# Kernel optimization log

Hardware: AMD Instinct MI355X
Metric: run time of the kernel (lower is better)

Reference implementation:

```python
import jax, jax.numpy as jnp
import numpy as np

# Dimensions
BATCH = 4
NUM_NODE = 20000
NUM_EDGE = 1280000   # avg degree 64
K = 2                # num_rd_kernels
NUM_SEQ = 13         # num_sequence (13 time points -> 12 intervals)
SEQ_IN = 12
RES = 2              # fixed-step Euler substeps per interval (resolution)
TEMP = 1.0           # temperature for gate softmax
NUM_OUT = -12        # num_output_sequence slice


def setup_inputs() -> dict:
    key = jax.random.key(0)
    ks = jax.random.split(key, 6)
    inputs = jax.random.normal(ks[0], (BATCH, 1, NUM_NODE, SEQ_IN), dtype=jnp.float32)
    gate = jax.random.normal(ks[1], (NUM_SEQ - 1, K), dtype=jnp.float32)
    # edge list from adjacency CSV (from/to columns)
    src = jax.random.randint(ks[2], (NUM_EDGE,), 0, NUM_NODE)
    dst = jax.random.randint(ks[3], (NUM_EDGE,), 0, NUM_NODE)
    # learned per-kernel parameters of multi_reaction_diffusion
    w = jax.random.normal(ks[4], (K, NUM_EDGE), dtype=jnp.float32) * 0.1  # edge diffusivity logits
    r = jax.random.normal(ks[5], (K, NUM_NODE), dtype=jnp.float32) * 0.1  # node reaction coeffs
    return {"inputs": inputs, "gate": gate, "w": w, "r": r, "src": src, "dst": dst}


def _dxdt(x, g, w, r, src, dst):
    # x: [B,N]  g: [K]  w: [K,E]  r: [K,N]
    a = jax.nn.sigmoid(w)                                   # [K,E] edge diffusivity
    xs = x[:, src]                                          # [B,E]
    xd = x[:, dst]                                          # [B,E]
    msg = a[:, None, :] * (xs - xd)[None, :, :]             # [K,B,E]
    # scatter-add messages into destination nodes
    diff = jax.ops.segment_sum(jnp.moveaxis(msg, 2, 0), dst, num_segments=NUM_NODE)  # [N,K,B]
    diff = jnp.transpose(diff, (1, 2, 0))                   # [K,B,N]
    react = r[:, None, :] * x[None] * (1.0 - x[None])       # [K,B,N] logistic reaction
    return jnp.einsum('k,kbn->bn', g, diff + react)         # gate-weighted mix of RD kernels


def reference(inputs, gate, w, r, src, dst):
    x0 = inputs[:, 0, :, -1]                                # [B,N]
    dt = 1.0 / (NUM_SEQ - 1)
    h = jnp.float32(dt / RES)
    gates = jax.nn.softmax(gate / TEMP, axis=-1)            # [NUM_SEQ-1, K]

    def interval(x, g):
        def step(xc, _):
            return xc + h * _dxdt(xc, g, w, r, src, dst), None
        x, _ = jax.lax.scan(step, x, None, length=RES)
        return x, x

    _, traj = jax.lax.scan(interval, x0, gates)             # [NUM_SEQ-1, B, N]
    out = jnp.concatenate([x0[None], traj], axis=0)         # [NUM_SEQ, B, N]
    return out[NUM_OUT:]                                    # last 12 horizons
```

## Files before the change

kernel.cpp:

```cpp
#include <hip/hip_runtime.h>
#include <hip/hip_fp16.h>
#include <math.h>

#define NNODE 20000
#define NEDGE 1280000
#define HSTEP (1.0f/24.0f)
#define NBUCK 313
#define CAP   4608
#define EPB   2048
#define NPB   40
#define TPB   320
#define NBLK  (NNODE/NPB)
#define CAPB  2976
#define NGRP  25
#define GSZ   20
#define XSTR  160256

#define GEPI(g)   (32*(g))
#define RCNTI(g)  (32*(25+(g)))
#define XARRI(x)  (32*(50+(x)))
#define XCNTI(x)  (32*(58+(x)))
#define MASTERI   (32*66)
#define RMASTERI  (32*67)

#define AGT __HIP_MEMORY_SCOPE_AGENT

__global__ void rd_init(const float* __restrict__ inp,
                        uint2* __restrict__ xh,
                        int* __restrict__ cursor,
                        int* __restrict__ bar) {
    int n = blockIdx.x * blockDim.x + threadIdx.x;
    if (n < NBUCK) cursor[n] = n * CAP;
    if (n < 2560) bar[n] = 0;
    if (n < NNODE) {
        float x0 = inp[0 * NNODE * 12 + n * 12 + 11];
        float x1 = inp[1 * NNODE * 12 + n * 12 + 11];
        float x2 = inp[2 * NNODE * 12 + n * 12 + 11];
        float x3 = inp[3 * NNODE * 12 + n * 12 + 11];
        __half2 lo = __floats2half2_rn(x0, x1);
        __half2 hi = __floats2half2_rn(x2, x3);
        uint2 st;
        st.x = *(unsigned*)&lo;
        st.y = *(unsigned*)&hi;
        xh[n] = st;
    }
}

__global__ __launch_bounds__(256) void rd_part(const int4* __restrict__ src4,
                                               const int4* __restrict__ dst4,
                                               const float4* __restrict__ w4,
                                               int* __restrict__ cursor,
                                               uint2* __restrict__ rec) {
    __shared__ int h[4][NBUCK];
    __shared__ uint4 cache[EPB / 4];
    int t = threadIdx.x, wv = t >> 6;
    for (int i = t; i < 4 * NBUCK; i += 256) ((int*)h)[i] = 0;
    __syncthreads();
    int q0 = blockIdx.x * (EPB / 4);
    #pragma unroll
    for (int k = 0; k < 2; ++k) {
        int qi = q0 + k * 256 + t;
        int4 d4 = dst4[qi];
        int dd[4] = {d4.x, d4.y, d4.z, d4.w};
        unsigned cc[4];
        #pragma unroll
        for (int u = 0; u < 4; ++u) {
            int rank = atomicAdd(&h[wv][dd[u] >> 6], 1);
            cc[u] = (unsigned)dd[u] | ((unsigned)rank << 15);
        }
        cache[k * 256 + t] = make_uint4(cc[0], cc[1], cc[2], cc[3]);
    }
    __syncthreads();
    for (int i = t; i < NBUCK; i += 256) {
        int c0 = h[0][i], c1 = h[1][i], c2 = h[2][i], c3 = h[3][i];
        int tot = c0 + c1 + c2 + c3;
        int gb = tot ? atomicAdd(&cursor[i], tot) : 0;
        h[0][i] = gb;
        h[1][i] = gb + c0;
        h[2][i] = gb + c0 + c1;
        h[3][i] = gb + c0 + c1 + c2;
    }
    __syncthreads();
    #pragma unroll
    for (int k = 0; k < 2; ++k) {
        int qi = q0 + k * 256 + t;
        int4 s4 = src4[qi];
        float4 wa = w4[qi];
        float4 wb = w4[NEDGE / 4 + qi];
        uint4 c4 = cache[k * 256 + t];
        int ss[4] = {s4.x, s4.y, s4.z, s4.w};
        float fa[4] = {wa.x, wa.y, wa.z, wa.w};
        float fb[4] = {wb.x, wb.y, wb.z, wb.w};
        unsigned cc[4] = {c4.x, c4.y, c4.z, c4.w};
        #pragma unroll
        for (int u = 0; u < 4; ++u) {
            int d = cc[u] & 0x7FFF;
            int rank = (int)(cc[u] >> 15);
            int b = d >> 6;
            int p = h[wv][b] + rank;
            float s0 = 1.0f / (1.0f + expf(-fa[u]));
            float s1 = 1.0f / (1.0f + expf(-fb[u]));
            __half2 hh = __floats2half2_rn(s0, s1);
            uint2 rq;
            rq.x = (unsigned)ss[u] | ((unsigned)(d & 63) << 16);
            rq.y = *(unsigned*)&hh;
            if (p < (b + 1) * CAP) rec[p] = rq;
        }
    }
}

__global__ void rd_bscan(const int* __restrict__ cursor, int* __restrict__ boff) {
    int lane = threadIdx.x;
    int carry = 0;
    #pragma unroll
    for (int c = 0; c < 5; ++c) {
        int i = c * 64 + lane;
        int v = (i < NBUCK) ? (cursor[i] - i * CAP) : 0;
        int incl = v;
        #pragma unroll
        for (int o = 1; o < 64; o <<= 1) {
            int u = __shfl_up(incl, o, 64);
            if (lane >= o) incl += u;
        }
        if (i < NBUCK) boff[i] = carry + incl - v;
        carry += __shfl(incl, 63, 64);
    }
    if (lane == 0) boff[NBUCK] = carry;
}

__global__ __launch_bounds__(512) void rd_bsort(const uint2* __restrict__ rec,
                                                const int* __restrict__ cursor,
                                                const int* __restrict__ boff,
                                                unsigned short* __restrict__ es16,
                                                unsigned* __restrict__ ew32,
                                                int* __restrict__ offsets) {
    __shared__ uint2 rs[CAP];
    __shared__ int h[64], excl[64];
    int b = blockIdx.x;
    int ib = b * CAP;
    int cnt = cursor[b] - ib; if (cnt > CAP) cnt = CAP;
    int ob = boff[b];
    if (threadIdx.x < 64) h[threadIdx.x] = 0;
    __syncthreads();
    for (int i = threadIdx.x; i < cnt; i += 512) {
        uint2 q = rec[ib + i];
        rs[i] = q;
        atomicAdd(&h[(q.x >> 16) & 63], 1);
    }
    __syncthreads();
    if (threadIdx.x < 64) {
        int lane = threadIdx.x;
        int v = h[lane];
        int incl = v;
        #pragma unroll
        for (int o = 1; o < 64; o <<= 1) {
            int u = __shfl_up(incl, o, 64);
            if (lane >= o) incl += u;
        }
        excl[lane] = incl - v;
        int n = b * 64 + lane;
        if (n < NNODE) offsets[n] = ob + excl[lane];
        h[lane] = 0;
    }
    if (b == NBUCK - 1 && threadIdx.x == 0) offsets[NNODE] = NEDGE;
    __syncthreads();
    for (int i = threadIdx.x; i < cnt; i += 512) {
        uint2 q = rs[i];
        int dl = (q.x >> 16) & 63;
        int rank = atomicAdd(&h[dl], 1);
        int p = ob + excl[dl] + rank;
        es16[p] = (unsigned short)(q.x & 0xFFFFu);
        ew32[p] = q.y;
    }
}

__global__ __launch_bounds__(TPB, 3) void rd_run(
        const float* __restrict__ inp, const uint2* __restrict__ x0h,
        char* __restrict__ recb,
        const unsigned short* __restrict__ es16,
        const unsigned* __restrict__ ew32,
        const int* __restrict__ offsets,
        const float* __restrict__ r, const float* __restrict__ gate,
        float* __restrict__ out, int* bar) {
    __shared__ uint2 lrec[CAPB];
    __shared__ int lofs[NPB + 1];
    __shared__ float lgate[24];
    int t = threadIdx.x;
    int n0 = blockIdx.x * NPB;
    if (t <= NPB) lofs[t] = offsets[n0 + t];
    if (t >= 64 && t < 88) lgate[t - 64] = gate[t - 64];
    __syncthreads();
    int ebase = lofs[0];
    int ecnt  = lofs[NPB] - ebase; if (ecnt > CAPB) ecnt = CAPB;
    for (int i = t; i < ecnt; i += TPB)
        lrec[i] = make_uint2((unsigned)es16[ebase + i], ew32[ebase + i]);
    int node = n0 + (t >> 3);
    int sub  = t & 7;
    float r0n = r[node], r1n = r[NNODE + node];
    float4 xreg;
    xreg.x = inp[0 * NNODE * 12 + node * 12 + 11];
    xreg.y = inp[1 * NNODE * 12 + node * 12 + 11];
    xreg.z = inp[2 * NNODE * 12 + node * 12 + 11];
    xreg.w = inp[3 * NNODE * 12 + node * 12 + 11];
    int jb = lofs[t >> 3] - ebase;
    int je = lofs[(t >> 3) + 1] - ebase;
    int grp = blockIdx.x / GSZ;

    int myxcd = 0, nx = 0, nxcd = 0;
    if (t == 0) {
        __builtin_amdgcn_fence(__ATOMIC_ACQUIRE, "agent");
        myxcd = (int)(__builtin_amdgcn_s_getreg(63508) & 0xF);
        __hip_atomic_fetch_add(&bar[XCNTI(myxcd)], 1, __ATOMIC_RELAXED, AGT);
        int rA = __hip_atomic_fetch_add(&bar[RCNTI(grp)], 1, __ATOMIC_RELEASE, AGT);
        if (rA == GSZ - 1) {
            int rm = __hip_atomic_fetch_add(&bar[RMASTERI], 1, __ATOMIC_RELAXED, AGT);
            if (rm == NGRP - 1)
                for (int g = 0; g < NGRP; ++g)
                    __hip_atomic_store(&bar[GEPI(g)], 1, __ATOMIC_RELAXED, AGT);
        }
        while (__hip_atomic_load(&bar[GEPI(grp)], __ATOMIC_RELAXED, AGT) < 1)
            __builtin_amdgcn_s_sleep(2);
        asm volatile("" ::: "memory");
        nx = __hip_atomic_load(&bar[XCNTI(myxcd)], __ATOMIC_RELAXED, AGT);
        for (int x2 = 0; x2 < 8; ++x2)
            nxcd += (__hip_atomic_load(&bar[XCNTI(x2)], __ATOMIC_RELAXED, AGT) > 0);
    }
    __syncthreads();

    float S0 = 0.f, S1 = 0.f;
    for (int j = jb + sub; j < je; j += 8) {
        uint2 q = lrec[j];
        float2 f = __half22float2(*(__half2*)&q.y);
        S0 += f.x; S1 += f.y;
    }
    #pragma unroll
    for (int m = 4; m >= 1; m >>= 1) {
        S0 += __shfl_xor(S0, m, 64);
        S1 += __shfl_xor(S1, m, 64);
    }

    for (int p = 0; p < 24; ++p) {
        int itv = p >> 1;
        float ga = lgate[2 * itv], gb = lgate[2 * itv + 1];
        float g0 = 1.0f / (1.0f + expf(gb - ga));
        float g1 = 1.0f - g0;
        float rc = fmaf(g0, r0n, g1 * r1n);
        float wsum = fmaf(g0, S0, g1 * S1);
        const uint2* xi = p ? (const uint2*)(recb + (size_t)(p - 1) * XSTR) : x0h;
        uint2*       xo = (uint2*)(recb + (size_t)p * XSTR);

        float4 acc = make_float4(0.f, 0.f, 0.f, 0.f);
        int j = jb + sub;
        for (; j + 56 < je; j += 64) {
            uint2 q0 = lrec[j],      q1 = lrec[j +  8], q2 = lrec[j + 16], q3 = lrec[j + 24];
            uint2 q4 = lrec[j + 32], q5 = lrec[j + 40], q6 = lrec[j + 48], q7 = lrec[j + 56];
            uint2 g0v = xi[q0.x], g1v = xi[q1.x], g2v = xi[q2.x], g3v = xi[q3.x];
            uint2 g4v = xi[q4.x], g5v = xi[q5.x], g6v = xi[q6.x], g7v = xi[q7.x];
            #define WE(qq) ({ float2 f_ = __half22float2(*(__half2*)&qq.y); fmaf(g0, f_.x, g1 * f_.y); })
            #define ACC4(gv, we) { \
                float2 lo_ = __half22float2(*(__half2*)&gv.x); \
                float2 hi_ = __half22float2(*(__half2*)&gv.y); \
                acc.x = fmaf(we, lo_.x, acc.x); \
                acc.y = fmaf(we, lo_.y, acc.y); \
                acc.z = fmaf(we, hi_.x, acc.z); \
                acc.w = fmaf(we, hi_.y, acc.w); }
            float we0 = WE(q0), we1 = WE(q1), we2 = WE(q2), we3 = WE(q3);
            float we4 = WE(q4), we5 = WE(q5), we6 = WE(q6), we7 = WE(q7);
            ACC4(g0v, we0) ACC4(g1v, we1) ACC4(g2v, we2) ACC4(g3v, we3)
            ACC4(g4v, we4) ACC4(g5v, we5) ACC4(g6v, we6) ACC4(g7v, we7)
        }
        if (j + 24 < je) {
            uint2 q0 = lrec[j], q1 = lrec[j + 8], q2 = lrec[j + 16], q3 = lrec[j + 24];
            uint2 g0v = xi[q0.x], g1v = xi[q1.x], g2v = xi[q2.x], g3v = xi[q3.x];
            float we0 = WE(q0), we1 = WE(q1), we2 = WE(q2), we3 = WE(q3);
            ACC4(g0v, we0) ACC4(g1v, we1) ACC4(g2v, we2) ACC4(g3v, we3)
            j += 32;
        }
        if (j + 8 < je) {
            uint2 q0 = lrec[j], q1 = lrec[j + 8];
            uint2 g0v = xi[q0.x], g1v = xi[q1.x];
            float we0 = WE(q0), we1 = WE(q1);
            ACC4(g0v, we0) ACC4(g1v, we1)
            j += 16;
        }
        if (j < je) {
            uint2 q0 = lrec[j];
            uint2 g0v = xi[q0.x];
            float we0 = WE(q0);
            ACC4(g0v, we0)
        }
        #pragma unroll
        for (int m = 4; m >= 1; m >>= 1) {
            acc.x += __shfl_xor(acc.x, m, 64);
            acc.y += __shfl_xor(acc.y, m, 64);
            acc.z += __shfl_xor(acc.z, m, 64);
            acc.w += __shfl_xor(acc.w, m, 64);
        }
        float4 xd = xreg;
        float4 xn;
        xn.x = xd.x + HSTEP * ((acc.x - wsum * xd.x) + rc * xd.x * (1.0f - xd.x));
        xn.y = xd.y + HSTEP * ((acc.y - wsum * xd.y) + rc * xd.y * (1.0f - xd.y));
        xn.z = xd.z + HSTEP * ((acc.z - wsum * xd.z) + rc * xd.z * (1.0f - xd.z));
        xn.w = xd.w + HSTEP * ((acc.w - wsum * xd.w) + rc * xd.w * (1.0f - xd.w));
        xreg = xn;
        if (sub == 0) {
            __half2 lo = __floats2half2_rn(xn.x, xn.y);
            __half2 hi = __floats2half2_rn(xn.z, xn.w);
            uint2 st;
            st.x = *(unsigned*)&lo;
            st.y = *(unsigned*)&hi;
            xo[node] = st;
        }
        if ((p & 1) && sub < 4) {
            float v = (sub == 0) ? xn.x : (sub == 1) ? xn.y : (sub == 2) ? xn.z : xn.w;
            out[(itv * 4 + sub) * NNODE + node] = v;
        }

        if (p < 23) {
            __syncthreads();
            if (t == 0) {
                int o = __hip_atomic_fetch_add(&bar[XARRI(myxcd)], 1,
                                               __ATOMIC_RELAXED, AGT);
                if (o == (p + 1) * nx - 1) {
                    __builtin_amdgcn_fence(__ATOMIC_RELEASE, "agent");
                    int om = __hip_atomic_fetch_add(&bar[MASTERI], 1,
                                                    __ATOMIC_RELAXED, AGT);
                    if (om == (p + 1) * nxcd - 1)
                        for (int g = 0; g < NGRP; ++g)
                            __hip_atomic_store(&bar[GEPI(g)], p + 2,
                                               __ATOMIC_RELAXED, AGT);
                }
                while (__hip_atomic_load(&bar[GEPI(grp)], __ATOMIC_RELAXED, AGT) < p + 2)
                    __builtin_amdgcn_s_sleep(2);
                asm volatile("" ::: "memory");
            }
            __syncthreads();
        }
    }
}

extern "C" void kernel_launch(void* const* d_in, const int* in_sizes, int n_in,
                              void* d_out, int out_size, void* d_ws, size_t ws_size,
                              hipStream_t stream) {
    const float* inp  = (const float*)d_in[0];
    const float* gate = (const float*)d_in[1];
    const float* w    = (const float*)d_in[2];
    const float* r    = (const float*)d_in[3];
    const int*   src  = (const int*)d_in[4];
    const int*   dst  = (const int*)d_in[5];
    float* out = (float*)d_out;

    char* ws = (char*)d_ws;
    uint2*          xH      = (uint2*) (ws + 0);
    int*            offsets = (int*)   (ws + 641024);
    int*            cursor  = (int*)   (ws + 721152);
    int*            boff    = (int*)   (ws + 722432);
    int*            bar     = (int*)   (ws + 723712);
    char*           recb    = (ws + 740096);
    unsigned short* es16    = (unsigned short*)(ws + 12278528);
    unsigned*       ew32    = (unsigned*)(ws + 14838528);

    rd_init <<<(NNODE + 255) / 256, 256, 0, stream>>>(inp, xH, cursor, bar);
    rd_part <<<NEDGE / EPB, 256, 0, stream>>>((const int4*)src, (const int4*)dst,
                                              (const float4*)w, cursor, (uint2*)recb);
    rd_bscan<<<1, 64, 0, stream>>>(cursor, boff);
    rd_bsort<<<NBUCK, 512, 0, stream>>>((const uint2*)recb, cursor, boff,
                                        es16, ew32, offsets);
    rd_run  <<<NBLK, TPB, 0, stream>>>(inp, xH, recb, es16, ew32, offsets,
                                       r, gate, out, bar);
}
```

Measured before the change: 234.2 us.

## Stage full node state in LDS per step and keep edges in registers

```diff
diff --git a/kernel.cpp b/kernel.cpp
--- a/kernel.cpp
+++ b/kernel.cpp
@@ -8,12 +8,11 @@
 #define NBUCK 313
 #define CAP   4608
 #define EPB   2048
-#define NPB   40
-#define TPB   320
+#define NPB   80
+#define TPB   640
 #define NBLK  (NNODE/NPB)
-#define CAPB  2976
 #define NGRP  25
-#define GSZ   20
+#define GSZ   10
 #define XSTR  160256
 
 #define GEPI(g)   (32*(g))
@@ -174,7 +173,7 @@
     }
 }
 
-__global__ __launch_bounds__(TPB, 3) void rd_run(
+__global__ __launch_bounds__(TPB, 1) void rd_run(
         const float* __restrict__ inp, const uint2* __restrict__ x0h,
         char* __restrict__ recb,
         const unsigned short* __restrict__ es16,
@@ -182,28 +181,28 @@
         const int* __restrict__ offsets,
         const float* __restrict__ r, const float* __restrict__ gate,
         float* __restrict__ out, int* bar) {
-    __shared__ uint2 lrec[CAPB];
-    __shared__ int lofs[NPB + 1];
+    __shared__ uint2 lds_x[NNODE];
     __shared__ float lgate[24];
     int t = threadIdx.x;
     int n0 = blockIdx.x * NPB;
-    if (t <= NPB) lofs[t] = offsets[n0 + t];
-    if (t >= 64 && t < 88) lgate[t - 64] = gate[t - 64];
-    __syncthreads();
-    int ebase = lofs[0];
-    int ecnt  = lofs[NPB] - ebase; if (ecnt > CAPB) ecnt = CAPB;
-    for (int i = t; i < ecnt; i += TPB)
-        lrec[i] = make_uint2((unsigned)es16[ebase + i], ew32[ebase + i]);
+    if (t < 24) lgate[t] = gate[t];
     int node = n0 + (t >> 3);
     int sub  = t & 7;
+    int jb = offsets[node], je = offsets[node + 1];
     float r0n = r[node], r1n = r[NNODE + node];
     float4 xreg;
     xreg.x = inp[0 * NNODE * 12 + node * 12 + 11];
     xreg.y = inp[1 * NNODE * 12 + node * 12 + 11];
     xreg.z = inp[2 * NNODE * 12 + node * 12 + 11];
     xreg.w = inp[3 * NNODE * 12 + node * 12 + 11];
-    int jb = lofs[t >> 3] - ebase;
-    int je = lofs[(t >> 3) + 1] - ebase;
+    unsigned ees[8], eew[8];
+    #pragma unroll
+    for (int k = 0; k < 8; ++k) {
+        int idx = jb + sub + 8 * k;
+        bool v = idx < je;
+        ees[k] = v ? (unsigned)es16[idx] : 0u;
+        eew[k] = v ? ew32[idx] : 0u;
+    }
     int grp = blockIdx.x / GSZ;
 
     int myxcd = 0, nx = 0, nxcd = 0;
@@ -228,9 +227,14 @@
     __syncthreads();
 
     float S0 = 0.f, S1 = 0.f;
-    for (int j = jb + sub; j < je; j += 8) {
-        uint2 q = lrec[j];
-        float2 f = __half22float2(*(__half2*)&q.y);
+    #pragma unroll
+    for (int k = 0; k < 8; ++k) {
+        float2 f = __half22float2(*(__half2*)&eew[k]);
+        S0 += f.x; S1 += f.y;
+    }
+    for (int j = jb + 64 + sub; j < je; j += 8) {
+        unsigned q = ew32[j];
+        float2 f = __half22float2(*(__half2*)&q);
         S0 += f.x; S1 += f.y;
     }
     #pragma unroll
@@ -238,6 +242,14 @@
         S0 += __shfl_xor(S0, m, 64);
         S1 += __shfl_xor(S1, m, 64);
     }
+
+    #define ACC4(gv, we) { \
+        float2 lo_ = __half22float2(*(__half2*)&gv.x); \
+        float2 hi_ = __half22float2(*(__half2*)&gv.y); \
+        acc.x = fmaf(we, lo_.x, acc.x); \
+        acc.y = fmaf(we, lo_.y, acc.y); \
+        acc.z = fmaf(we, hi_.x, acc.z); \
+        acc.w = fmaf(we, hi_.y, acc.w); }
 
     for (int p = 0; p < 24; ++p) {
         int itv = p >> 1;
@@ -246,48 +258,31 @@
         float g1 = 1.0f - g0;
         float rc = fmaf(g0, r0n, g1 * r1n);
         float wsum = fmaf(g0, S0, g1 * S1);
-        const uint2* xi = p ? (const uint2*)(recb + (size_t)(p - 1) * XSTR) : x0h;
-        uint2*       xo = (uint2*)(recb + (size_t)p * XSTR);
+        const uint2* xprev = p ? (const uint2*)(recb + (size_t)(p - 1) * XSTR) : x0h;
+        uint2*       xo    = (uint2*)(recb + (size_t)p * XSTR);
+
+        {
+            const uint4* s4 = (const uint4*)xprev;
+            uint4* l4 = (uint4*)lds_x;
+            for (int i = t; i < NNODE / 2; i += TPB) l4[i] = s4[i];
+        }
+        __syncthreads();
 
         float4 acc = make_float4(0.f, 0.f, 0.f, 0.f);
-        int j = jb + sub;
-        for (; j + 56 < je; j += 64) {
-            uint2 q0 = lrec[j],      q1 = lrec[j +  8], q2 = lrec[j + 16], q3 = lrec[j + 24];
-            uint2 q4 = lrec[j + 32], q5 = lrec[j + 40], q6 = lrec[j + 48], q7 = lrec[j + 56];
-            uint2 g0v = xi[q0.x], g1v = xi[q1.x], g2v = xi[q2.x], g3v = xi[q3.x];
-            uint2 g4v = xi[q4.x], g5v = xi[q5.x], g6v = xi[q6.x], g7v = xi[q7.x];
-            #define WE(qq) ({ float2 f_ = __half22float2(*(__half2*)&qq.y); fmaf(g0, f_.x, g1 * f_.y); })
-            #define ACC4(gv, we) { \
-                float2 lo_ = __half22float2(*(__half2*)&gv.x); \
-                float2 hi_ = __half22float2(*(__half2*)&gv.y); \
-                acc.x = fmaf(we, lo_.x, acc.x); \
-                acc.y = fmaf(we, lo_.y, acc.y); \
-                acc.z = fmaf(we, hi_.x, acc.z); \
-                acc.w = fmaf(we, hi_.y, acc.w); }
-            float we0 = WE(q0), we1 = WE(q1), we2 = WE(q2), we3 = WE(q3);
-            float we4 = WE(q4), we5 = WE(q5), we6 = WE(q6), we7 = WE(q7);
-            ACC4(g0v, we0) ACC4(g1v, we1) ACC4(g2v, we2) ACC4(g3v, we3)
-            ACC4(g4v, we4) ACC4(g5v, we5) ACC4(g6v, we6) ACC4(g7v, we7)
-        }
-        if (j + 24 < je) {
-            uint2 q0 = lrec[j], q1 = lrec[j + 8], q2 = lrec[j + 16], q3 = lrec[j + 24];
-            uint2 g0v = xi[q0.x], g1v = xi[q1.x], g2v = xi[q2.x], g3v = xi[q3.x];
-            float we0 = WE(q0), we1 = WE(q1), we2 = WE(q2), we3 = WE(q3);
-            ACC4(g0v, we0) ACC4(g1v, we1) ACC4(g2v, we2) ACC4(g3v, we3)
-            j += 32;
-        }
-        if (j + 8 < je) {
-            uint2 q0 = lrec[j], q1 = lrec[j + 8];
-            uint2 g0v = xi[q0.x], g1v = xi[q1.x];
-            float we0 = WE(q0), we1 = WE(q1);
-            ACC4(g0v, we0) ACC4(g1v, we1)
-            j += 16;
-        }
-        if (j < je) {
-            uint2 q0 = lrec[j];
-            uint2 g0v = xi[q0.x];
-            float we0 = WE(q0);
-            ACC4(g0v, we0)
+        #pragma unroll
+        for (int k = 0; k < 8; ++k) {
+            uint2 gv = lds_x[ees[k]];
+            float2 f = __half22float2(*(__half2*)&eew[k]);
+            float we = fmaf(g0, f.x, g1 * f.y);
+            ACC4(gv, we)
+        }
+        for (int j = jb + 64 + sub; j < je; j += 8) {
+            unsigned s = (unsigned)es16[j];
+            unsigned q = ew32[j];
+            uint2 gv = lds_x[s];
+            float2 f = __half22float2(*(__half2*)&q);
+            float we = fmaf(g0, f.x, g1 * f.y);
+            ACC4(gv, we)
         }
         #pragma unroll
         for (int m = 4; m >= 1; m >>= 1) {
```

Measured after the change: 238.1 us. Within noise of the previous version (+1.7%).
